# Performance work log

Hardware: AMD Instinct MI355X
Metric: run time of the kernel (lower is better)

Reference implementation:

```python
import jax, jax.numpy as jnp
import numpy as np
from jax import lax

SEQ_LEN = 5000
C_IN = 12
KERNEL_LEN = 9
NUM_KERNELS = 10000
BATCH = 16


def _get_dilations(seq_len, kernel_length):
    max_d = (seq_len - 1) // (kernel_length - 1)
    d, out = 1, []
    while d <= max_d:
        out.append(d)
        d *= 2
    return out if out else [1]

DILATIONS = _get_dilations(SEQ_LEN, KERNEL_LEN)  # [1,2,...,512], 10 dilations
KPD = NUM_KERNELS // len(DILATIONS)              # 1000 kernels per dilation


def setup_inputs() -> dict:
    key = jax.random.key(0)
    kx, kw, kb = jax.random.split(key, 3)
    x = jax.random.normal(kx, (BATCH, C_IN, SEQ_LEN), dtype=jnp.float32)
    # ternary {-1,0,1} MiniRocket weights, one [KPD, C_IN, 9] bank per dilation
    weights = jax.random.randint(kw, (len(DILATIONS), KPD, C_IN, KERNEL_LEN), -1, 2).astype(jnp.float32)
    biases = jax.random.normal(kb, (len(DILATIONS), KPD), dtype=jnp.float32) * 0.1
    return {"x": x, "weights": weights, "biases": biases}


def reference(x, weights, biases):
    # x: [B, C_in, L]; weights: [D, KPD, C_in, 9]; biases: [D, KPD]
    feats = []
    for i, d in enumerate(DILATIONS):
        # 'same' padding: total pad = d*(9-1) = 8d (even), split 4d/4d -> SAME
        out = lax.conv_general_dilated(
            x, weights[i],
            window_strides=(1,), padding='SAME', rhs_dilation=(d,),
            dimension_numbers=('NCH', 'OIH', 'NCH'))  # [B, KPD, L]
        maxv = out.max(axis=-1)                                        # [B, KPD]
        ppv = (out > biases[i][None, :, None]).astype(x.dtype).mean(axis=-1)  # [B, KPD]
        feats.append(maxv)
        feats.append(ppv)
    return jnp.concatenate(feats, axis=1)  # [B, 2*NUM_KERNELS]
```

## Files before the change

kernel.cpp:

```cpp
#include <hip/hip_runtime.h>
#include <cstdint>
#include <cstddef>

#define SEQ 5000
#define CIN 12
#define KL 9
#define ND 10
#define KPD 1000
#define NB 16
#define KPAD 128
#define NKP 1024
#define BM 64
#define SPB 79
#define STRIP_US (BM * KPAD)
#define QS 20

typedef __attribute__((ext_vector_type(4))) float f32x4;
typedef __attribute__((ext_vector_type(8))) __bf16 bf16x8;
typedef __attribute__((ext_vector_type(8))) unsigned short u16x8;

__device__ __forceinline__ unsigned fkey(float f) {
    unsigned u = __float_as_uint(f);
    return (u & 0x80000000u) ? ~u : (u | 0x80000000u);
}
__device__ __forceinline__ float unfkey(unsigned k) {
    unsigned u = (k & 0x80000000u) ? (k ^ 0x80000000u) : ~k;
    return __uint_as_float(u);
}
__device__ __forceinline__ unsigned short f2bf(float f) {
    unsigned u = __float_as_uint(f);
    u += 0x7fffu + ((u >> 16) & 1u);
    return (unsigned short)(u >> 16);
}

__global__ __launch_bounds__(256) void wprep(const float* __restrict__ w,
                                             unsigned short* __restrict__ wbf) {
    const int i = blockIdx.x * 256 + threadIdx.x;
    if (i >= ND * NKP * KPAD) return;
    const int kk   = i & (KPAD - 1);
    const int krow = (i >> 7) & (NKP - 1);
    const int di   = i >> 17;
    float v = 0.f;
    if (krow < KPD && kk < CIN * KL)
        v = w[((size_t)di * KPD + krow) * (CIN * KL) + kk];
    wbf[i] = f2bf(v);
}

__global__ __launch_bounds__(256) void im2col(const float* __restrict__ x,
                                              unsigned short* __restrict__ Aim,
                                              int g0) {
    const int s  = blockIdx.x;
    const int b  = blockIdx.y;
    const int dl = blockIdx.z;
    const int d  = 1 << (g0 + dl);
    const int tid  = threadIdx.x;
    const int lane = tid & 63;
    const int wv   = tid >> 6;

    __shared__ __align__(16) unsigned short sb[STRIP_US];

    const float* xb = x + (size_t)b * CIN * SEQ;
    const int t0 = s * BM;
    const int t  = t0 + lane;
    const int base = t - 4 * d;
    const bool rowvalid = (t < SEQ);

#pragma unroll
    for (int cwi = 0; cwi < 4; ++cwi) {
        const int cw = wv * 4 + cwi;
        u16x8 pk;
        int cc = cw * 8;
        int c = cc / 9, j = cc - c * 9;
#pragma unroll
        for (int e = 0; e < 8; ++e) {
            const int idx = base + j * d;
            float v = 0.f;
            if (rowvalid && cc < CIN * KL && idx >= 0 && idx < SEQ)
                v = xb[c * SEQ + idx];
            pk[e] = f2bf(v);
            ++cc; if (++j == KL) { j = 0; ++c; }
        }
        *(u16x8*)(sb + lane * KPAD + ((cw * 8) ^ ((lane & 7) << 3))) = pk;
    }
    __syncthreads();

    unsigned short* outp = Aim + ((size_t)(dl * NB + b) * SPB + s) * STRIP_US;
#pragma unroll
    for (int i = 0; i < 4; ++i) {
        const int u = (i * 256 + tid) * 8;
        *(u16x8*)(outp + u) = *(const u16x8*)(sb + u);
    }
}

__global__ __launch_bounds__(256, 4) void mr_gemm(
    const unsigned short* __restrict__ Aim,
    const unsigned short* __restrict__ wbf,
    const float* __restrict__ bias,
    unsigned* __restrict__ gkey, unsigned* __restrict__ gcnt, int g0)
{
    __shared__ __align__(16) unsigned short lA[2][STRIP_US];

    const int phys = blockIdx.x;
    const int gg   = ((phys >> 6) << 3) | (phys & 7);
    const int ksub = (phys >> 3) & 7;
    const int q  = gg & 3;
    const int b  = (gg >> 2) & 15;
    const int dl = gg >> 6;
    const int di = g0 + dl;

    const int tid  = threadIdx.x;
    const int lane = tid & 63;
    const int wv   = tid >> 6;
    const int fr   = lane & 15;
    const int ks   = lane >> 4;

    const int sBeg = q * QS;
    const int sEnd = (q == 3) ? SPB : (sBeg + QS);

    const unsigned short* Ab = Aim + (size_t)(dl * NB + b) * SPB * STRIP_US;
    const unsigned short* wd = wbf + (size_t)di * NKP * KPAD;
    const int kc0 = ksub * 128 + wv * 32 + fr;
    const int kc1 = kc0 + 16;
    const unsigned short* wp = wd + (size_t)kc0 * KPAD + ks * 8;

    bf16x8 b0[4], b1[4];
#pragma unroll
    for (int kk = 0; kk < 4; ++kk) {
        b0[kk] = *(const bf16x8*)(wp + kk * 32);
        b1[kk] = *(const bf16x8*)(wp + 16 * KPAD + kk * 32);
    }
    const float* bb = bias + (size_t)di * KPD;
    const float bv0 = (kc0 < KPD) ? bb[kc0] : 3.0e38f;
    const float bv1 = (kc1 < KPD) ? bb[kc1] : 3.0e38f;

    float rmax0 = -3.0e38f, rmax1 = -3.0e38f;
    unsigned rcnt0 = 0, rcnt1 = 0;

    int abase[4];
#pragma unroll
    for (int m = 0; m < 4; ++m) {
        const int row = m * 16 + fr;
        abase[m] = row * 256 + ((ks * 16) ^ ((row & 7) << 4));
    }

    {
        const char* src = (const char*)(Ab + (size_t)sBeg * STRIP_US) + wv * 4096 + lane * 16;
        char* dst = (char*)&lA[0][0] + wv * 4096;
#pragma unroll
        for (int i = 0; i < 4; ++i)
            __builtin_amdgcn_global_load_lds(
                (const __attribute__((address_space(1))) unsigned int*)(src + i * 1024),
                (__attribute__((address_space(3))) unsigned int*)(dst + i * 1024),
                16, 0, 0);
    }
    __syncthreads();

    for (int s = sBeg; s < sEnd; ++s) {
        const int cur = (s - sBeg) & 1;
        if (s + 1 < sEnd) {
            const char* src = (const char*)(Ab + (size_t)(s + 1) * STRIP_US) + wv * 4096 + lane * 16;
            char* dst = (char*)&lA[cur ^ 1][0] + wv * 4096;
#pragma unroll
            for (int i = 0; i < 4; ++i)
                __builtin_amdgcn_global_load_lds(
                    (const __attribute__((address_space(1))) unsigned int*)(src + i * 1024),
                    (__attribute__((address_space(3))) unsigned int*)(dst + i * 1024),
                    16, 0, 0);
        }

        const char* bufc = (const char*)&lA[cur][0];
        f32x4 acc0[4], acc1[4];
#pragma unroll
        for (int m = 0; m < 4; ++m) {
            acc0[m] = (f32x4){0.f, 0.f, 0.f, 0.f};
            acc1[m] = (f32x4){0.f, 0.f, 0.f, 0.f};
        }
#pragma unroll
        for (int m = 0; m < 4; ++m) {
            const char* pa0 = bufc + abase[m];
            const char* pa1 = bufc + (abase[m] ^ 64);
#pragma unroll
            for (int kk = 0; kk < 4; ++kk) {
                const char* p = (kk & 1) ? pa1 : pa0;
                const bf16x8 a = *(const bf16x8*)(p + (kk >> 1) * 128);
                acc0[m] = __builtin_amdgcn_mfma_f32_16x16x32_bf16(a, b0[kk], acc0[m], 0, 0, 0);
                acc1[m] = __builtin_amdgcn_mfma_f32_16x16x32_bf16(a, b1[kk], acc1[m], 0, 0, 0);
            }
        }

        if (s != SPB - 1) {
            float m0 = -3.0e38f, m1 = -3.0e38f;
            unsigned c0 = 0, c1 = 0;
#pragma unroll
            for (int m = 0; m < 4; ++m) {
#pragma unroll
                for (int r = 0; r < 4; ++r) {
                    const float x0 = acc0[m][r], x1 = acc1[m][r];
                    m0 = fmaxf(m0, x0); c0 += (x0 > bv0) ? 1u : 0u;
                    m1 = fmaxf(m1, x1); c1 += (x1 > bv1) ? 1u : 0u;
                }
            }
            rmax0 = fmaxf(rmax0, m0); rcnt0 += c0;
            rmax1 = fmaxf(rmax1, m1); rcnt1 += c1;
        } else {
            if (ks < 2) {
#pragma unroll
                for (int r = 0; r < 4; ++r) {
                    const float x0 = acc0[0][r], x1 = acc1[0][r];
                    rmax0 = fmaxf(rmax0, x0); rcnt0 += (x0 > bv0) ? 1u : 0u;
                    rmax1 = fmaxf(rmax1, x1); rcnt1 += (x1 > bv1) ? 1u : 0u;
                }
            }
        }
        __syncthreads();
    }

    rmax0 = fmaxf(rmax0, __shfl_xor(rmax0, 16, 64));
    rcnt0 += (unsigned)__shfl_xor((int)rcnt0, 16, 64);
    rmax0 = fmaxf(rmax0, __shfl_xor(rmax0, 32, 64));
    rcnt0 += (unsigned)__shfl_xor((int)rcnt0, 32, 64);
    rmax1 = fmaxf(rmax1, __shfl_xor(rmax1, 16, 64));
    rcnt1 += (unsigned)__shfl_xor((int)rcnt1, 16, 64);
    rmax1 = fmaxf(rmax1, __shfl_xor(rmax1, 32, 64));
    rcnt1 += (unsigned)__shfl_xor((int)rcnt1, 32, 64);

    if (lane < 16) {
        const size_t slotbase = ((size_t)b * ND + di) * KPD;
        if (kc0 < KPD) {
            atomicMax(&gkey[slotbase + kc0], fkey(rmax0));
            atomicAdd(&gcnt[slotbase + kc0], rcnt0);
        }
        if (kc1 < KPD) {
            atomicMax(&gkey[slotbase + kc1], fkey(rmax1));
            atomicAdd(&gcnt[slotbase + kc1], rcnt1);
        }
    }
}

__global__ __launch_bounds__(256) void mr_fin(
    const unsigned* __restrict__ gkey, const unsigned* __restrict__ gcnt,
    float* __restrict__ out)
{
    const int i = blockIdx.x * 256 + threadIdx.x;
    if (i >= NB * ND * KPD) return;
    const int k  = i % KPD;
    const int di = (i / KPD) % ND;
    const int b  = i / (KPD * ND);
    const float maxv = unfkey(gkey[i]);
    const float ppv  = (float)gcnt[i] * (1.0f / (float)SEQ);
    float* ob = out + (size_t)b * (2 * ND * KPD);
    ob[di * 2 * KPD + k]       = maxv;
    ob[di * 2 * KPD + KPD + k] = ppv;
}

extern "C" void kernel_launch(void* const* d_in, const int* in_sizes, int n_in,
                              void* d_out, int out_size, void* d_ws, size_t ws_size,
                              hipStream_t stream) {
    const float* x    = (const float*)d_in[0];
    const float* w    = (const float*)d_in[1];
    const float* bias = (const float*)d_in[2];
    float* out = (float*)d_out;

    const size_t statsB = (size_t)NB * ND * KPD * 4;
    const size_t wbfB   = (size_t)ND * NKP * KPAD * 2;
    unsigned* gkey = (unsigned*)d_ws;
    unsigned* gcnt = (unsigned*)((char*)d_ws + statsB);
    unsigned short* wbf = (unsigned short*)((char*)d_ws + 2 * statsB);
    unsigned short* Aim = (unsigned short*)((char*)d_ws + 2 * statsB + wbfB);

    const size_t perDil = (size_t)NB * SPB * STRIP_US * 2;
    const size_t head = 2 * statsB + wbfB;
    size_t avail = (ws_size > head) ? (ws_size - head) : 0;
    int NG = (int)(avail / perDil);
    if (NG > ND) NG = ND;
    if (NG < 1) NG = 1;

    hipMemsetAsync(d_ws, 0, 2 * statsB, stream);

    const int wtot = ND * NKP * KPAD;
    wprep<<<(wtot + 255) / 256, 256, 0, stream>>>(w, wbf);

    for (int g0 = 0; g0 < ND; g0 += NG) {
        const int ng = (ND - g0 < NG) ? (ND - g0) : NG;
        im2col<<<dim3(SPB, NB, ng), 256, 0, stream>>>(x, Aim, g0);
        mr_gemm<<<ng * 512, 256, 0, stream>>>(Aim, wbf, bias, gkey, gcnt, g0);
    }

    const int tot = NB * ND * KPD;
    mr_fin<<<(tot + 255) / 256, 256, 0, stream>>>(gkey, gcnt, out);
}
```

Baseline: 284.6 us.

## Widen GEMM N-tile per wave to 64 kernels, halving grid and A reloads

Each wave now computes four 16-column MFMA tiles (64 kernels) instead of two, so each block covers 256 kernels and the grid shrinks from 8 to 4 k-subsets per (dilation, batch, quarter). Every A fragment read from LDS feeds four MFMAs, which halves the im2col strip traffic from global memory to LDS and the LDS reads per MFMA. Block indexing also changes so that ksub is the slowest-varying index. The cost is more registers for weights and accumulators (64 accumulator VGPRs plus 64 for B fragments), which can lower occupancy under launch_bounds(256,4), and fewer blocks in flight.

```diff
diff --git a/kernel.cpp b/kernel.cpp
--- a/kernel.cpp
+++ b/kernel.cpp
@@ -96,16 +96,17 @@
     const unsigned short* __restrict__ Aim,
     const unsigned short* __restrict__ wbf,
     const float* __restrict__ bias,
-    unsigned* __restrict__ gkey, unsigned* __restrict__ gcnt, int g0)
+    unsigned* __restrict__ gkey, unsigned* __restrict__ gcnt,
+    int g0, int nrest)
 {
     __shared__ __align__(16) unsigned short lA[2][STRIP_US];
 
     const int phys = blockIdx.x;
-    const int gg   = ((phys >> 6) << 3) | (phys & 7);
-    const int ksub = (phys >> 3) & 7;
-    const int q  = gg & 3;
-    const int b  = (gg >> 2) & 15;
-    const int dl = gg >> 6;
+    const int ksub = phys / nrest;
+    const int rest = phys - ksub * nrest;
+    const int q  = rest & 3;
+    const int b  = (rest >> 2) & 15;
+    const int dl = rest >> 6;
     const int di = g0 + dl;
 
     const int tid  = threadIdx.x;
@@ -119,22 +120,28 @@
 
     const unsigned short* Ab = Aim + (size_t)(dl * NB + b) * SPB * STRIP_US;
     const unsigned short* wd = wbf + (size_t)di * NKP * KPAD;
-    const int kc0 = ksub * 128 + wv * 32 + fr;
-    const int kc1 = kc0 + 16;
-    const unsigned short* wp = wd + (size_t)kc0 * KPAD + ks * 8;
-
-    bf16x8 b0[4], b1[4];
-#pragma unroll
-    for (int kk = 0; kk < 4; ++kk) {
-        b0[kk] = *(const bf16x8*)(wp + kk * 32);
-        b1[kk] = *(const bf16x8*)(wp + 16 * KPAD + kk * 32);
-    }
+    const int kcb = ksub * 256 + wv * 64 + fr;
+    const unsigned short* wp = wd + (size_t)kcb * KPAD + ks * 8;
     const float* bb = bias + (size_t)di * KPD;
-    const float bv0 = (kc0 < KPD) ? bb[kc0] : 3.0e38f;
-    const float bv1 = (kc1 < KPD) ? bb[kc1] : 3.0e38f;
-
-    float rmax0 = -3.0e38f, rmax1 = -3.0e38f;
-    unsigned rcnt0 = 0, rcnt1 = 0;
+
+    float bv[4];
+#pragma unroll
+    for (int n = 0; n < 4; ++n) {
+        const int kc = kcb + n * 16;
+        bv[n] = (kc < KPD) ? bb[kc] : 3.0e38f;
+    }
+
+    bf16x8 bfr[4][4];
+#pragma unroll
+    for (int n = 0; n < 4; ++n)
+#pragma unroll
+        for (int kk = 0; kk < 4; ++kk)
+            bfr[n][kk] = *(const bf16x8*)(wp + (size_t)(n * 16) * KPAD + kk * 32);
+
+    float rmax[4];
+    unsigned rcnt[4];
+#pragma unroll
+    for (int n = 0; n < 4; ++n) { rmax[n] = -3.0e38f; rcnt[n] = 0; }
 
     int abase[4];
 #pragma unroll
@@ -169,12 +176,13 @@
         }
 
         const char* bufc = (const char*)&lA[cur][0];
-        f32x4 acc0[4], acc1[4];
-#pragma unroll
-        for (int m = 0; m < 4; ++m) {
-            acc0[m] = (f32x4){0.f, 0.f, 0.f, 0.f};
-            acc1[m] = (f32x4){0.f, 0.f, 0.f, 0.f};
-        }
+        f32x4 acc[4][4];
+#pragma unroll
+        for (int m = 0; m < 4; ++m)
+#pragma unroll
+            for (int n = 0; n < 4; ++n)
+                acc[m][n] = (f32x4){0.f, 0.f, 0.f, 0.f};
+
 #pragma unroll
         for (int m = 0; m < 4; ++m) {
             const char* pa0 = bufc + abase[m];
@@ -183,56 +191,63 @@
             for (int kk = 0; kk < 4; ++kk) {
                 const char* p = (kk & 1) ? pa1 : pa0;
                 const bf16x8 a = *(const bf16x8*)(p + (kk >> 1) * 128);
-                acc0[m] = __builtin_amdgcn_mfma_f32_16x16x32_bf16(a, b0[kk], acc0[m], 0, 0, 0);
-                acc1[m] = __builtin_amdgcn_mfma_f32_16x16x32_bf16(a, b1[kk], acc1[m], 0, 0, 0);
+#pragma unroll
+                for (int n = 0; n < 4; ++n)
+                    acc[m][n] = __builtin_amdgcn_mfma_f32_16x16x32_bf16(
+                        a, bfr[n][kk], acc[m][n], 0, 0, 0);
             }
         }
 
         if (s != SPB - 1) {
-            float m0 = -3.0e38f, m1 = -3.0e38f;
-            unsigned c0 = 0, c1 = 0;
-#pragma unroll
-            for (int m = 0; m < 4; ++m) {
-#pragma unroll
-                for (int r = 0; r < 4; ++r) {
-                    const float x0 = acc0[m][r], x1 = acc1[m][r];
-                    m0 = fmaxf(m0, x0); c0 += (x0 > bv0) ? 1u : 0u;
-                    m1 = fmaxf(m1, x1); c1 += (x1 > bv1) ? 1u : 0u;
+#pragma unroll
+            for (int n = 0; n < 4; ++n) {
+                float m0 = -3.0e38f;
+                unsigned c0 = 0;
+#pragma unroll
+                for (int m = 0; m < 4; ++m) {
+#pragma unroll
+                    for (int r = 0; r < 4; ++r) {
+                        const float x0 = acc[m][n][r];
+                        m0 = fmaxf(m0, x0);
+                        c0 += (x0 > bv[n]) ? 1u : 0u;
+                    }
+                }
+                rmax[n] = fmaxf(rmax[n], m0);
+                rcnt[n] += c0;
+            }
+        } else {
+            if (ks < 2) {
+#pragma unroll
+                for (int n = 0; n < 4; ++n) {
+#pragma unroll
+                    for (int r = 0; r < 4; ++r) {
+                        const float x0 = acc[0][n][r];
+                        rmax[n] = fmaxf(rmax[n], x0);
+                        rcnt[n] += (x0 > bv[n]) ? 1u : 0u;
+                    }
                 }
             }
-            rmax0 = fmaxf(rmax0, m0); rcnt0 += c0;
-            rmax1 = fmaxf(rmax1, m1); rcnt1 += c1;
-        } else {
-            if (ks < 2) {
-#pragma unroll
-                for (int r = 0; r < 4; ++r) {
-                    const float x0 = acc0[0][r], x1 = acc1[0][r];
-                    rmax0 = fmaxf(rmax0, x0); rcnt0 += (x0 > bv0) ? 1u : 0u;
-                    rmax1 = fmaxf(rmax1, x1); rcnt1 += (x1 > bv1) ? 1u : 0u;
-                }
-            }
         }
         __syncthreads();
     }
 
-    rmax0 = fmaxf(rmax0, __shfl_xor(rmax0, 16, 64));
-    rcnt0 += (unsigned)__shfl_xor((int)rcnt0, 16, 64);
-    rmax0 = fmaxf(rmax0, __shfl_xor(rmax0, 32, 64));
-    rcnt0 += (unsigned)__shfl_xor((int)rcnt0, 32, 64);
-    rmax1 = fmaxf(rmax1, __shfl_xor(rmax1, 16, 64));
-    rcnt1 += (unsigned)__shfl_xor((int)rcnt1, 16, 64);
-    rmax1 = fmaxf(rmax1, __shfl_xor(rmax1, 32, 64));
-    rcnt1 += (unsigned)__shfl_xor((int)rcnt1, 32, 64);
+#pragma unroll
+    for (int n = 0; n < 4; ++n) {
+        rmax[n] = fmaxf(rmax[n], __shfl_xor(rmax[n], 16, 64));
+        rcnt[n] += (unsigned)__shfl_xor((int)rcnt[n], 16, 64);
+        rmax[n] = fmaxf(rmax[n], __shfl_xor(rmax[n], 32, 64));
+        rcnt[n] += (unsigned)__shfl_xor((int)rcnt[n], 32, 64);
+    }
 
     if (lane < 16) {
         const size_t slotbase = ((size_t)b * ND + di) * KPD;
-        if (kc0 < KPD) {
-            atomicMax(&gkey[slotbase + kc0], fkey(rmax0));
-            atomicAdd(&gcnt[slotbase + kc0], rcnt0);
-        }
-        if (kc1 < KPD) {
-            atomicMax(&gkey[slotbase + kc1], fkey(rmax1));
-            atomicAdd(&gcnt[slotbase + kc1], rcnt1);
+#pragma unroll
+        for (int n = 0; n < 4; ++n) {
+            const int kc = kcb + n * 16;
+            if (kc < KPD) {
+                atomicMax(&gkey[slotbase + kc], fkey(rmax[n]));
+                atomicAdd(&gcnt[slotbase + kc], rcnt[n]);
+            }
         }
     }
 }
@@ -283,7 +298,8 @@
     for (int g0 = 0; g0 < ND; g0 += NG) {
         const int ng = (ND - g0 < NG) ? (ND - g0) : NG;
         im2col<<<dim3(SPB, NB, ng), 256, 0, stream>>>(x, Aim, g0);
-        mr_gemm<<<ng * 512, 256, 0, stream>>>(Aim, wbf, bias, gkey, gcnt, g0);
+        const int nrest = ng * 64;
+        mr_gemm<<<4 * nrest, 256, 0, stream>>>(Aim, wbf, bias, gkey, gcnt, g0, nrest);
     }
 
     const int tot = NB * ND * KPD;
```

Measured after the change: 963.4 us. +238.5%, slower.
